# Optimization experiments

Hardware: AMD Instinct MI355X
Metric: run time of the kernel (lower is better)

The kernel has to match this reference:

```python
import jax, jax.numpy as jnp
import numpy as np

N = 4096
IN_F = 256
OUT_F = 128
K = 3
BETA = 0.5
ALPHA = 0.2  # leaky relu negative slope
NEG_BIG = -9e15


def setup_inputs() -> dict:
    key = jax.random.key(0)
    k1, k2, k3, k4 = jax.random.split(key, 4)
    h = jax.random.normal(k1, (N, IN_F), dtype=jnp.float32)
    k_mask_list = jax.random.randint(k2, (K, N, N), 0, 2, dtype=jnp.int32)
    # xavier_uniform with gain=1.414
    def xavier(k, shape, gain=1.414):
        fan_in, fan_out = shape[0], shape[1]
        bound = gain * np.sqrt(6.0 / (fan_in + fan_out))
        return jax.random.uniform(k, shape, jnp.float32, -bound, bound)
    W = xavier(k3, (IN_F * K, OUT_F))
    a = xavier(k4, (2 * OUT_F * K, 1))
    return {"h": h, "k_mask_list": k_mask_list, "W": W, "a": a}


def reference(h, k_mask_list, W, a):
    # dropout p=0.0 / eval mode -> identity
    Wh = None
    for i in range(K - 1, -1, -1):
        Whnew = h @ W[i * IN_F:(i + 1) * IN_F, :]              # [N, OUT_F]
        if i == K - 1:
            Wh = Whnew
        a1 = a[2 * i * OUT_F:(2 * i + 1) * OUT_F, :]           # [OUT_F, 1]
        a2 = a[(2 * i + 1) * OUT_F:(2 * i + 2) * OUT_F, :]     # [OUT_F, 1]
        Wh1 = Whnew @ a1                                        # [N, 1]
        Wh2 = Whnew @ a2                                        # [N, 1]
        e = jax.nn.leaky_relu(Wh1 + Wh2.T, negative_slope=ALPHA)  # [N, N]
        masked = jnp.where(k_mask_list[i] > 0, e, NEG_BIG)
        attention = jax.nn.softmax(masked, axis=1)              # [N, N]
        Wh = (1.0 - BETA) * (attention @ Whnew) + BETA * Wh
    return jax.nn.elu(Wh)  # concat=True
```

## Files before the change

### kernel.cpp

```cpp
#include <hip/hip_runtime.h>
#include <hip/hip_bf16.h>

#define NN 4096
#define IN_F 256
#define OUT_F 128
#define ALPHA 0.2f

typedef __bf16 bf16x8 __attribute__((ext_vector_type(8)));
typedef float f32x4 __attribute__((ext_vector_type(4)));
typedef float f32x16 __attribute__((ext_vector_type(16)));

__device__ __forceinline__ unsigned short f2bf(float f) {
  union { float f; unsigned int u; } x; x.f = f;
  unsigned int r = x.u + 0x7FFF + ((x.u >> 16) & 1);
  return (unsigned short)(r >> 16);
}

__global__ __launch_bounds__(256) void k_cvt_w(const float* __restrict__ W,
                                               unsigned short* __restrict__ Wtb) {
  const int i = blockIdx.y;
  const int k0 = blockIdx.x * 32;
  const int t = threadIdx.x;
  __shared__ float tile[32][129];
  #pragma unroll
  for (int j = 0; j < 16; ++j) {
    int idx = t + j * 256;
    int r = idx >> 7, c = idx & 127;
    tile[r][c] = W[(size_t)(i * IN_F + k0 + r) * OUT_F + c];
  }
  __syncthreads();
  const int c = t >> 1, half = t & 1;
  unsigned short* dst = Wtb + ((size_t)i * OUT_F + c) * IN_F + k0 + half * 16;
  #pragma unroll
  for (int g = 0; g < 4; ++g) {
    ushort4 v;
    v.x = f2bf(tile[half * 16 + g * 4 + 0][c]);
    v.y = f2bf(tile[half * 16 + g * 4 + 1][c]);
    v.z = f2bf(tile[half * 16 + g * 4 + 2][c]);
    v.w = f2bf(tile[half * 16 + g * 4 + 3][c]);
    *(ushort4*)(dst + g * 4) = v;
  }
}

__global__ __launch_bounds__(256) void k_front(const float* __restrict__ h,
                                               const unsigned short* __restrict__ Wtb,
                                               const float* __restrict__ a,
                                               float* __restrict__ Whnew2,
                                               unsigned short* __restrict__ Vopt,
                                               float* __restrict__ Wh1,
                                               float* __restrict__ Wh2,
                                               unsigned short* __restrict__ ew2pb,
                                               unsigned short* __restrict__ ew2mb,
                                               float* __restrict__ gmax2) {
  const int i = blockIdx.y;
  const int r0 = blockIdx.x * 32;
  const int t = threadIdx.x;
  const int lane = t & 63, wid = t >> 6;
  const int m = wid & 1, nh = wid >> 1, nbase = nh * 64;
  const int ln = lane & 15, lk = lane >> 4;

  __shared__ float a1s[128], a2s[128];
  __shared__ float red1[2][32], red2[2][32];
  __shared__ float ewsp[32], ewsm[32];
  __shared__ unsigned short T[2][32][130];

  if (t < 128) {
    a1s[t] = a[(size_t)2 * i * OUT_F + t];
    a2s[t] = a[(size_t)(2 * i + 1) * OUT_F + t];
  }
  __syncthreads();

  const float* ap = h + (size_t)(r0 + m * 16 + ln) * IN_F + lk * 8;
  const unsigned short* bp = Wtb + ((size_t)i * OUT_F + nbase + ln) * IN_F + lk * 8;

  f32x4 z4 = {0.f, 0.f, 0.f, 0.f};
  f32x4 acc[4] = {z4, z4, z4, z4};
  #pragma unroll
  for (int ks = 0; ks < 8; ++ks) {
    float4 h0 = *(const float4*)(ap + ks * 32);
    float4 h1 = *(const float4*)(ap + ks * 32 + 4);
    union { unsigned short u[8]; bf16x8 v; } av;
    av.u[0] = f2bf(h0.x); av.u[1] = f2bf(h0.y); av.u[2] = f2bf(h0.z); av.u[3] = f2bf(h0.w);
    av.u[4] = f2bf(h1.x); av.u[5] = f2bf(h1.y); av.u[6] = f2bf(h1.z); av.u[7] = f2bf(h1.w);
    acc[0] = __builtin_amdgcn_mfma_f32_16x16x32_bf16(av.v, *(const bf16x8*)(bp + 0 * 16 * IN_F + ks * 32), acc[0], 0, 0, 0);
    acc[1] = __builtin_amdgcn_mfma_f32_16x16x32_bf16(av.v, *(const bf16x8*)(bp + 1 * 16 * IN_F + ks * 32), acc[1], 0, 0, 0);
    acc[2] = __builtin_amdgcn_mfma_f32_16x16x32_bf16(av.v, *(const bf16x8*)(bp + 2 * 16 * IN_F + ks * 32), acc[2], 0, 0, 0);
    acc[3] = __builtin_amdgcn_mfma_f32_16x16x32_bf16(av.v, *(const bf16x8*)(bp + 3 * 16 * IN_F + ks * 32), acc[3], 0, 0, 0);
  }

  float d1[4] = {0.f, 0.f, 0.f, 0.f}, d2[4] = {0.f, 0.f, 0.f, 0.f};
  #pragma unroll
  for (int f = 0; f < 4; ++f) {
    const int col = nbase + f * 16 + ln;
    const float va1 = a1s[col], va2 = a2s[col];
    #pragma unroll
    for (int q = 0; q < 4; ++q) {
      const float v = acc[f][q];
      d1[q] += v * va1;
      d2[q] += v * va2;
    }
  }
  #pragma unroll
  for (int msk = 1; msk < 16; msk <<= 1) {
    #pragma unroll
    for (int q = 0; q < 4; ++q) {
      d1[q] += __shfl_xor(d1[q], msk, 64);
      d2[q] += __shfl_xor(d2[q], msk, 64);
    }
  }
  if (ln == 0) {
    #pragma unroll
    for (int q = 0; q < 4; ++q) {
      red1[nh][m * 16 + lk * 4 + q] = d1[q];
      red2[nh][m * 16 + lk * 4 + q] = d2[q];
    }
  }
  if (i == 2) {
    #pragma unroll
    for (int f = 0; f < 4; ++f) {
      const int col = nbase + f * 16 + ln;
      #pragma unroll
      for (int q = 0; q < 4; ++q)
        Whnew2[(size_t)(r0 + m * 16 + lk * 4 + q) * OUT_F + col] = acc[f][q];
    }
  }
  __syncthreads();

  if (t < 32) {
    const float w1 = red1[0][t] + red1[1][t];
    const float w2 = red2[0][t] + red2[1][t];
    Wh1[(size_t)i * NN + r0 + t] = w1;
    Wh2[(size_t)i * NN + r0 + t] = w2;
    const float ep = __expf(w2), em = __expf(ALPHA * w2);
    ewsp[t] = ep; ewsm[t] = em;
    ew2pb[(size_t)i * NN + r0 + t] = f2bf(ep);
    ew2mb[(size_t)i * NN + r0 + t] = f2bf(em);
    float mv = w2;
    #pragma unroll
    for (int o = 16; o > 0; o >>= 1) mv = fmaxf(mv, __shfl_down(mv, o, 32));
    if (t == 0 && mv > 0.f)
      atomicMax((int*)gmax2 + i, __float_as_int(mv));
  }
  __syncthreads();

  #pragma unroll
  for (int f = 0; f < 4; ++f) {
    const int n = nbase + f * 16 + ln;
    #pragma unroll
    for (int q = 0; q < 4; ++q) {
      const int c = m * 16 + lk * 4 + q;
      const float v = acc[f][q];
      T[0][c][n] = f2bf(ewsp[c] * v);
      T[1][c][n] = f2bf(ewsm[c] * v);
    }
  }
  __syncthreads();

  const int n = t & 127, ks = t >> 7;
  const int kslab = (r0 >> 4) + ks;
  #pragma unroll
  for (int s = 0; s < 2; ++s) {
    union { unsigned short u[16]; uint4 q[2]; } o;
    #pragma unroll
    for (int j = 0; j < 16; ++j) o.u[j] = T[s][ks * 16 + j][n];
    unsigned short* dst = Vopt + (((size_t)(i * 2 + s) * 256 + kslab) * 128 + n) * 16;
    *(uint4*)(dst) = o.q[0];
    *(uint4*)(dst + 8) = o.q[1];
  }
}

__global__ __launch_bounds__(256) void k_heavy(const unsigned short* __restrict__ Vopt,
                                               const int* __restrict__ mask,
                                               const float* __restrict__ Wh1,
                                               const float* __restrict__ Wh2,
                                               const unsigned short* __restrict__ ew2pb,
                                               const unsigned short* __restrict__ ew2mb,
                                               const float* __restrict__ gmax2,
                                               float* __restrict__ Upart,
                                               float* __restrict__ SPp,
                                               float* __restrict__ SMp) {
  const unsigned int lid = blockIdx.x + 64u * (blockIdx.y + 3u * blockIdx.z);
  const unsigned int swz = (lid & 7u) * 96u + (lid >> 3);
  const int bx = swz & 63;
  const int w = swz >> 6;
  const int i = w % 3;
  const int z = w / 3;

  const int r0 = bx * 64;
  const int cb = z * 1024;
  const int t = threadIdx.x, lane = t & 63, wid = t >> 6;
  const int m = wid & 1, nh = wid >> 1;
  const int l31 = lane & 31, kh = lane >> 5;
  const int n0 = nh * 64 + l31, n1 = n0 + 32;

  const int myrow = r0 + m * 32 + l31;
  const float w1 = Wh1[(size_t)i * NN + myrow];
  const int* mrow = mask + ((size_t)i * NN + myrow) * NN + cb + kh * 8;
  const float* w2p = Wh2 + (size_t)i * NN + cb + kh * 8;

  const size_t fragoff = (size_t)nh * 1024 + l31 * 16 + kh * 8;
  const unsigned short* vP = Vopt + ((size_t)(i * 2 + 0) * 256 + (cb >> 4)) * 2048 + fragoff;
  const unsigned short* vM = Vopt + ((size_t)(i * 2 + 1) * 256 + (cb >> 4)) * 2048 + fragoff;
  const unsigned short* eB = (nh == 0 ? ew2pb : ew2mb) + (size_t)i * NN + cb + kh * 8;

  f32x16 accP0 = {}, accP1 = {}, accM0 = {}, accM1 = {}, accS = {};

  #pragma unroll 2
  for (int kslab = 0; kslab < 64; ++kslab) {
    const int ks16 = kslab * 16;
    int4 ma = *(const int4*)(mrow + ks16);
    int4 mb = *(const int4*)(mrow + ks16 + 4);
    float4 wa = *(const float4*)(w2p + ks16);
    float4 wb = *(const float4*)(w2p + ks16 + 4);

    union { unsigned int u[4]; bf16x8 v; } aP, aM;
    {
      int mv[8] = {ma.x, ma.y, ma.z, ma.w, mb.x, mb.y, mb.z, mb.w};
      float wv[8] = {wa.x, wa.y, wa.z, wa.w, wb.x, wb.y, wb.z, wb.w};
      #pragma unroll
      for (int e = 0; e < 4; ++e) {
        const bool m0 = mv[2 * e] > 0,   p0 = (w1 + wv[2 * e]) > 0.f;
        const bool m1 = mv[2 * e + 1] > 0, p1 = (w1 + wv[2 * e + 1]) > 0.f;
        aP.u[e] = ((m0 && p0) ? 0x3F80u : 0u) | ((m1 && p1) ? 0x3F800000u : 0u);
        aM.u[e] = ((m0 && !p0) ? 0x3F80u : 0u) | ((m1 && !p1) ? 0x3F800000u : 0u);
      }
    }
    bf16x8 bP0 = *(const bf16x8*)(vP + (size_t)kslab * 2048);
    bf16x8 bP1 = *(const bf16x8*)(vP + (size_t)kslab * 2048 + 512);
    bf16x8 bM0 = *(const bf16x8*)(vM + (size_t)kslab * 2048);
    bf16x8 bM1 = *(const bf16x8*)(vM + (size_t)kslab * 2048 + 512);
    bf16x8 eF  = *(const bf16x8*)(eB + ks16);
    accP0 = __builtin_amdgcn_mfma_f32_32x32x16_bf16(aP.v, bP0, accP0, 0, 0, 0);
    accP1 = __builtin_amdgcn_mfma_f32_32x32x16_bf16(aP.v, bP1, accP1, 0, 0, 0);
    accM0 = __builtin_amdgcn_mfma_f32_32x32x16_bf16(aM.v, bM0, accM0, 0, 0, 0);
    accM1 = __builtin_amdgcn_mfma_f32_32x32x16_bf16(aM.v, bM1, accM1, 0, 0, 0);
    accS  = __builtin_amdgcn_mfma_f32_32x32x16_bf16(nh == 0 ? aP.v : aM.v, eF, accS, 0, 0, 0);
  }

  const float gi = gmax2[i];
  const int rbase = r0 + m * 32;
  #pragma unroll
  for (int q = 0; q < 16; ++q) {
    const int crow = (q & 3) + 8 * (q >> 2) + 4 * kh;
    const int r = rbase + crow;
    const float rw1 = Wh1[(size_t)i * NN + r];
    const float e0 = rw1 + gi;
    const float mx = (e0 > 0.f) ? e0 : ALPHA * e0;
    const float fp = __expf(rw1 - mx);
    const float fm = __expf(ALPHA * rw1 - mx);
    float* urow = Upart + ((size_t)(z * 3 + i) * NN + r) * OUT_F;
    urow[n0] = fp * accP0[q] + fm * accM0[q];
    urow[n1] = fp * accP1[q] + fm * accM1[q];
  }
  if (l31 == 0) {
    #pragma unroll
    for (int q = 0; q < 16; ++q) {
      const int r = rbase + (q & 3) + 8 * (q >> 2) + 4 * kh;
      if (nh == 0) SPp[(size_t)(z * 3 + i) * NN + r] = accS[q];
      else         SMp[(size_t)(z * 3 + i) * NN + r] = accS[q];
    }
  }
}

__global__ __launch_bounds__(256) void k_final(const float* __restrict__ Upart,
                                               const float* __restrict__ SPp,
                                               const float* __restrict__ SMp,
                                               const float* __restrict__ Wh1,
                                               const float* __restrict__ gmax2,
                                               const float* __restrict__ Whnew2,
                                               float* __restrict__ out) {
  int idx = blockIdx.x * 256 + threadIdx.x;
  int r = idx >> 7;
  float v = 0.125f * Whnew2[idx];
  #pragma unroll
  for (int i = 0; i < 3; ++i) {
    const float coef = (i == 0) ? 0.5f : (i == 1) ? 0.25f : 0.125f;
    const float w1 = Wh1[(size_t)i * NN + r];
    const float gi = gmax2[i];
    const float e0 = w1 + gi;
    const float mx = (e0 > 0.f) ? e0 : ALPHA * e0;
    const float fp = __expf(w1 - mx);
    const float fm = __expf(ALPHA * w1 - mx);
    float u = 0.f, sp = 0.f, sm = 0.f;
    #pragma unroll
    for (int zz = 0; zz < 4; ++zz) {
      u  += Upart[((size_t)(zz * 3 + i) * NN) * OUT_F + idx];
      sp += SPp[(size_t)(zz * 3 + i) * NN + r];
      sm += SMp[(size_t)(zz * 3 + i) * NN + r];
    }
    const float S = fp * sp + fm * sm;
    v += coef * u / S;
  }
  out[idx] = (v > 0.f) ? v : (__expf(v) - 1.0f);
}

extern "C" void kernel_launch(void* const* d_in, const int* in_sizes, int n_in,
                              void* d_out, int out_size, void* d_ws, size_t ws_size,
                              hipStream_t stream) {
  const float* h    = (const float*)d_in[0];
  const int*   mask = (const int*)d_in[1];
  const float* W    = (const float*)d_in[2];
  const float* a    = (const float*)d_in[3];
  float* out = (float*)d_out;

  float* Whnew2 = (float*)d_ws;
  float* Wh1    = Whnew2 + (size_t)NN * OUT_F;
  float* Wh2    = Wh1 + 3 * NN;
  float* gmax2  = Wh2 + 3 * NN;
  float* Upart  = gmax2 + 4;
  float* SPp    = Upart + (size_t)4 * 3 * NN * OUT_F;
  float* SMp    = SPp + 4 * 3 * NN;
  unsigned short* Wtb   = (unsigned short*)(SMp + 4 * 3 * NN);
  unsigned short* Vopt  = Wtb + (size_t)3 * OUT_F * IN_F;
  unsigned short* ew2pb = Vopt + (size_t)3 * 2 * 256 * 128 * 16;
  unsigned short* ew2mb = ew2pb + 3 * NN;

  hipMemsetAsync(gmax2, 0, 4 * sizeof(float), stream);
  k_cvt_w<<<dim3(8, 3), 256, 0, stream>>>(W, Wtb);
  k_front<<<dim3(128, 3), 256, 0, stream>>>(h, Wtb, a, Whnew2, Vopt, Wh1, Wh2, ew2pb, ew2mb, gmax2);
  k_heavy<<<dim3(64, 3, 4), 256, 0, stream>>>(Vopt, mask, Wh1, Wh2, ew2pb, ew2mb, gmax2, Upart, SPp, SMp);
  k_final<<<(NN * OUT_F) / 256, 256, 0, stream>>>(Upart, SPp, SMp, Wh1, gmax2, Whnew2, out);
}
```

Before: 398.0 us.

## Precompute mask sign bits cooperatively into LDS before MFMA loop

Each block now reads its 64x1024 mask tile once with coalesced row-wise loads. It computes the positive/negative leaky-relu selection as packed bits and stores them in shared memory. The MFMA loop then expands the bits into bf16 one-hot fragments from LDS. This removes duplicate mask reads by both column-half waves and the strided per-lane mask accesses. The cost is a serialized prologue with a barrier, so mask loading no longer overlaps with MFMA work.

```diff
diff --git a/kernel.cpp b/kernel.cpp
--- a/kernel.cpp
+++ b/kernel.cpp
@@ -14,6 +14,16 @@
   union { float f; unsigned int u; } x; x.f = f;
   unsigned int r = x.u + 0x7FFF + ((x.u >> 16) & 1);
   return (unsigned short)(r >> 16);
+}
+__device__ __forceinline__ bf16x8 bits2bf8(unsigned int b) {
+  union { unsigned int u[4]; bf16x8 v; } o;
+  #pragma unroll
+  for (int e = 0; e < 4; ++e) {
+    unsigned int lo = (b >> (2 * e)) & 1u;
+    unsigned int hi = (b >> (2 * e + 1)) & 1u;
+    o.u[e] = lo * 0x3F80u + hi * 0x3F800000u;
+  }
+  return o.v;
 }
 
 __global__ __launch_bounds__(256) void k_cvt_w(const float* __restrict__ W,
@@ -193,48 +203,62 @@
   const int l31 = lane & 31, kh = lane >> 5;
   const int n0 = nh * 64 + l31, n1 = n0 + 32;
 
-  const int myrow = r0 + m * 32 + l31;
-  const float w1 = Wh1[(size_t)i * NN + myrow];
-  const int* mrow = mask + ((size_t)i * NN + myrow) * NN + cb + kh * 8;
-  const float* w2p = Wh2 + (size_t)i * NN + cb + kh * 8;
+  __shared__ unsigned int bitsLDS[64][65];
+
+  const int wq = t >> 6;
+  const int cg = t & 63;
+  float w2v[16];
+  {
+    const float* w2b = Wh2 + (size_t)i * NN + cb + cg * 16;
+    #pragma unroll
+    for (int g = 0; g < 4; ++g) {
+      float4 f = *(const float4*)(w2b + g * 4);
+      w2v[g * 4 + 0] = f.x; w2v[g * 4 + 1] = f.y;
+      w2v[g * 4 + 2] = f.z; w2v[g * 4 + 3] = f.w;
+    }
+  }
+  const int* mcol = mask + ((size_t)i * NN + r0) * NN + cb + cg * 16;
+  #pragma unroll 2
+  for (int jj = 0; jj < 16; ++jj) {
+    const int rl = jj * 4 + wq;
+    const float w1r = Wh1[(size_t)i * NN + r0 + rl];
+    const int* mp = mcol + (size_t)rl * NN;
+    unsigned int bpk = 0, bmk = 0;
+    #pragma unroll
+    for (int g = 0; g < 4; ++g) {
+      int4 mv = *(const int4*)(mp + g * 4);
+      if (mv.x > 0) { if (w1r + w2v[g * 4 + 0] > 0.f) bpk |= 1u << (g * 4 + 0); else bmk |= 1u << (g * 4 + 0); }
+      if (mv.y > 0) { if (w1r + w2v[g * 4 + 1] > 0.f) bpk |= 1u << (g * 4 + 1); else bmk |= 1u << (g * 4 + 1); }
+      if (mv.z > 0) { if (w1r + w2v[g * 4 + 2] > 0.f) bpk |= 1u << (g * 4 + 2); else bmk |= 1u << (g * 4 + 2); }
+      if (mv.w > 0) { if (w1r + w2v[g * 4 + 3] > 0.f) bpk |= 1u << (g * 4 + 3); else bmk |= 1u << (g * 4 + 3); }
+    }
+    bitsLDS[rl][cg] = bpk | (bmk << 16);
+  }
+  __syncthreads();
 
   const size_t fragoff = (size_t)nh * 1024 + l31 * 16 + kh * 8;
   const unsigned short* vP = Vopt + ((size_t)(i * 2 + 0) * 256 + (cb >> 4)) * 2048 + fragoff;
   const unsigned short* vM = Vopt + ((size_t)(i * 2 + 1) * 256 + (cb >> 4)) * 2048 + fragoff;
   const unsigned short* eB = (nh == 0 ? ew2pb : ew2mb) + (size_t)i * NN + cb + kh * 8;
+  const int arow = m * 32 + l31;
 
   f32x16 accP0 = {}, accP1 = {}, accM0 = {}, accM1 = {}, accS = {};
 
   #pragma unroll 2
-  for (int kslab = 0; kslab < 64; ++kslab) {
-    const int ks16 = kslab * 16;
-    int4 ma = *(const int4*)(mrow + ks16);
-    int4 mb = *(const int4*)(mrow + ks16 + 4);
-    float4 wa = *(const float4*)(w2p + ks16);
-    float4 wb = *(const float4*)(w2p + ks16 + 4);
-
-    union { unsigned int u[4]; bf16x8 v; } aP, aM;
-    {
-      int mv[8] = {ma.x, ma.y, ma.z, ma.w, mb.x, mb.y, mb.z, mb.w};
-      float wv[8] = {wa.x, wa.y, wa.z, wa.w, wb.x, wb.y, wb.z, wb.w};
-      #pragma unroll
-      for (int e = 0; e < 4; ++e) {
-        const bool m0 = mv[2 * e] > 0,   p0 = (w1 + wv[2 * e]) > 0.f;
-        const bool m1 = mv[2 * e + 1] > 0, p1 = (w1 + wv[2 * e + 1]) > 0.f;
-        aP.u[e] = ((m0 && p0) ? 0x3F80u : 0u) | ((m1 && p1) ? 0x3F800000u : 0u);
-        aM.u[e] = ((m0 && !p0) ? 0x3F80u : 0u) | ((m1 && !p1) ? 0x3F800000u : 0u);
-      }
-    }
-    bf16x8 bP0 = *(const bf16x8*)(vP + (size_t)kslab * 2048);
-    bf16x8 bP1 = *(const bf16x8*)(vP + (size_t)kslab * 2048 + 512);
-    bf16x8 bM0 = *(const bf16x8*)(vM + (size_t)kslab * 2048);
-    bf16x8 bM1 = *(const bf16x8*)(vM + (size_t)kslab * 2048 + 512);
-    bf16x8 eF  = *(const bf16x8*)(eB + ks16);
-    accP0 = __builtin_amdgcn_mfma_f32_32x32x16_bf16(aP.v, bP0, accP0, 0, 0, 0);
-    accP1 = __builtin_amdgcn_mfma_f32_32x32x16_bf16(aP.v, bP1, accP1, 0, 0, 0);
-    accM0 = __builtin_amdgcn_mfma_f32_32x32x16_bf16(aM.v, bM0, accM0, 0, 0, 0);
-    accM1 = __builtin_amdgcn_mfma_f32_32x32x16_bf16(aM.v, bM1, accM1, 0, 0, 0);
-    accS  = __builtin_amdgcn_mfma_f32_32x32x16_bf16(nh == 0 ? aP.v : aM.v, eF, accS, 0, 0, 0);
+  for (int ks = 0; ks < 64; ++ks) {
+    const unsigned int wv = bitsLDS[arow][ks];
+    bf16x8 aP = bits2bf8((wv >> (kh * 8)) & 0xFFu);
+    bf16x8 aM = bits2bf8((wv >> (16 + kh * 8)) & 0xFFu);
+    bf16x8 bP0 = *(const bf16x8*)(vP + (size_t)ks * 2048);
+    bf16x8 bP1 = *(const bf16x8*)(vP + (size_t)ks * 2048 + 512);
+    bf16x8 bM0 = *(const bf16x8*)(vM + (size_t)ks * 2048);
+    bf16x8 bM1 = *(const bf16x8*)(vM + (size_t)ks * 2048 + 512);
+    bf16x8 eF  = *(const bf16x8*)(eB + ks * 16);
+    accP0 = __builtin_amdgcn_mfma_f32_32x32x16_bf16(aP, bP0, accP0, 0, 0, 0);
+    accP1 = __builtin_amdgcn_mfma_f32_32x32x16_bf16(aP, bP1, accP1, 0, 0, 0);
+    accM0 = __builtin_amdgcn_mfma_f32_32x32x16_bf16(aM, bM0, accM0, 0, 0, 0);
+    accM1 = __builtin_amdgcn_mfma_f32_32x32x16_bf16(aM, bM1, accM1, 0, 0, 0);
+    accS  = __builtin_amdgcn_mfma_f32_32x32x16_bf16(nh == 0 ? aP : aM, eF, accS, 0, 0, 0);
   }
 
   const float gi = gmax2[i];
```

Measured after the change: 396.7 us. No clear change (-0.3%).

## Precompute mask sign bits into LDS and stage V tiles with double buffering

Applied to the files above, without the earlier changes.

The heavy kernel now uses 512-thread blocks covering 128 rows by 512 columns. It first reads the int32 mask and the Wh1+Wh2 sign into a packed 8-bit-per-4-columns bit table in LDS, then streams the V slabs through double-buffered LDS staging shared by all warps instead of each warp loading them from global memory. The column split doubles to 8 partitions, so the final reduction and the workspace grow. This is meant to cut redundant global V loads and take mask decoding out of the MFMA loop, at the cost of extra syncthreads and more partial-sum traffic.

```diff
diff --git a/kernel.cpp b/kernel.cpp
--- a/kernel.cpp
+++ b/kernel.cpp
@@ -5,6 +5,8 @@
 #define IN_F 256
 #define OUT_F 128
 #define ALPHA 0.2f
+#define ROWS 128
+#define WCOLS 512
 
 typedef __bf16 bf16x8 __attribute__((ext_vector_type(8)));
 typedef float f32x4 __attribute__((ext_vector_type(4)));
@@ -169,76 +171,128 @@
   }
 }
 
-__global__ __launch_bounds__(256) void k_heavy(const unsigned short* __restrict__ Vopt,
-                                               const int* __restrict__ mask,
-                                               const float* __restrict__ Wh1,
-                                               const float* __restrict__ Wh2,
-                                               const unsigned short* __restrict__ ew2pb,
-                                               const unsigned short* __restrict__ ew2mb,
-                                               const float* __restrict__ gmax2,
-                                               float* __restrict__ Upart,
-                                               float* __restrict__ SPp,
-                                               float* __restrict__ SMp) {
-  const unsigned int lid = blockIdx.x + 64u * (blockIdx.y + 3u * blockIdx.z);
+__global__ __launch_bounds__(512, 4) void k_heavy(const unsigned short* __restrict__ Vopt,
+                                                  const int* __restrict__ mask,
+                                                  const float* __restrict__ Wh1,
+                                                  const float* __restrict__ Wh2,
+                                                  const unsigned short* __restrict__ ew2pb,
+                                                  const unsigned short* __restrict__ ew2mb,
+                                                  const float* __restrict__ gmax2,
+                                                  float* __restrict__ Upart,
+                                                  float* __restrict__ SPp,
+                                                  float* __restrict__ SMp) {
+  const unsigned int lid = blockIdx.x + 32u * (blockIdx.y + 3u * blockIdx.z);
   const unsigned int swz = (lid & 7u) * 96u + (lid >> 3);
-  const int bx = swz & 63;
-  const int w = swz >> 6;
+  const int bx = swz & 31;
+  const int w = swz >> 5;
   const int i = w % 3;
   const int z = w / 3;
 
-  const int r0 = bx * 64;
-  const int cb = z * 1024;
-  const int t = threadIdx.x, lane = t & 63, wid = t >> 6;
-  const int m = wid & 1, nh = wid >> 1;
+  const int r0 = bx * ROWS;
+  const int cb = z * WCOLS;
+  const int t = threadIdx.x;
+  const int lane = t & 63, wid = t >> 6;
+  const int g = wid & 3, nh = wid >> 2;
   const int l31 = lane & 31, kh = lane >> 5;
   const int n0 = nh * 64 + l31, n1 = n0 + 32;
 
-  const int myrow = r0 + m * 32 + l31;
-  const float w1 = Wh1[(size_t)i * NN + myrow];
-  const int* mrow = mask + ((size_t)i * NN + myrow) * NN + cb + kh * 8;
-  const float* w2p = Wh2 + (size_t)i * NN + cb + kh * 8;
-
-  const size_t fragoff = (size_t)nh * 1024 + l31 * 16 + kh * 8;
-  const unsigned short* vP = Vopt + ((size_t)(i * 2 + 0) * 256 + (cb >> 4)) * 2048 + fragoff;
-  const unsigned short* vM = Vopt + ((size_t)(i * 2 + 1) * 256 + (cb >> 4)) * 2048 + fragoff;
-  const unsigned short* eB = (nh == 0 ? ew2pb : ew2mb) + (size_t)i * NN + cb + kh * 8;
-
+  __shared__ unsigned char bits8[ROWS][132];
+  __shared__ unsigned short Vl[2][2][2][2048];
+  __shared__ unsigned short ews[2][WCOLS];
+
+  const int sg_st = wid >> 2;
+  const int q4 = wid & 3;
+  const unsigned short* myWin = Vopt + ((size_t)(i * 2 + sg_st) * 256 + (cb >> 4)) * 2048;
+  uint4 stg0, stg1;
+
+  {
+    const unsigned short* src = myWin + q4 * 1024 + lane * 8;
+    stg0 = *(const uint4*)(src);
+    stg1 = *(const uint4*)(src + 512);
+  }
+
+  if (t < WCOLS) {
+    ews[0][t] = ew2pb[(size_t)i * NN + cb + t];
+    ews[1][t] = ew2mb[(size_t)i * NN + cb + t];
+  }
+
+  {
+    const float* w2base = Wh2 + (size_t)i * NN + cb;
+    float4 w2a = *(const float4*)(w2base + lane * 4);
+    float4 w2b = *(const float4*)(w2base + 256 + lane * 4);
+    const int* mbase = mask + ((size_t)i * NN + r0) * NN + cb;
+    for (int p = 0; p < 16; ++p) {
+      const int r = p * 8 + wid;
+      const float w1 = Wh1[(size_t)i * NN + r0 + r];
+      const int* mp = mbase + (size_t)r * NN;
+      int4 ma = *(const int4*)(mp + lane * 4);
+      int4 mb = *(const int4*)(mp + 256 + lane * 4);
+      unsigned int b0 = 0, b1 = 0;
+      if (ma.x > 0) { if (w1 + w2a.x > 0.f) b0 |= 1u;  else b0 |= 16u; }
+      if (ma.y > 0) { if (w1 + w2a.y > 0.f) b0 |= 2u;  else b0 |= 32u; }
+      if (ma.z > 0) { if (w1 + w2a.z > 0.f) b0 |= 4u;  else b0 |= 64u; }
+      if (ma.w > 0) { if (w1 + w2a.w > 0.f) b0 |= 8u;  else b0 |= 128u; }
+      if (mb.x > 0) { if (w1 + w2b.x > 0.f) b1 |= 1u;  else b1 |= 16u; }
+      if (mb.y > 0) { if (w1 + w2b.y > 0.f) b1 |= 2u;  else b1 |= 32u; }
+      if (mb.z > 0) { if (w1 + w2b.z > 0.f) b1 |= 4u;  else b1 |= 64u; }
+      if (mb.w > 0) { if (w1 + w2b.w > 0.f) b1 |= 8u;  else b1 |= 128u; }
+      bits8[r][lane] = (unsigned char)b0;
+      bits8[r][64 + lane] = (unsigned char)b1;
+    }
+  }
+
+  __syncthreads();
+  {
+    unsigned short* dst = &Vl[0][sg_st][0][0] + q4 * 1024 + lane * 8;
+    *(uint4*)dst = stg0;
+    *(uint4*)(dst + 512) = stg1;
+  }
+  __syncthreads();
+
+  const int arow = g * 32 + l31;
   f32x16 accP0 = {}, accP1 = {}, accM0 = {}, accM1 = {}, accS = {};
 
-  #pragma unroll 2
-  for (int kslab = 0; kslab < 64; ++kslab) {
-    const int ks16 = kslab * 16;
-    int4 ma = *(const int4*)(mrow + ks16);
-    int4 mb = *(const int4*)(mrow + ks16 + 4);
-    float4 wa = *(const float4*)(w2p + ks16);
-    float4 wb = *(const float4*)(w2p + ks16 + 4);
-
-    union { unsigned int u[4]; bf16x8 v; } aP, aM;
-    {
-      int mv[8] = {ma.x, ma.y, ma.z, ma.w, mb.x, mb.y, mb.z, mb.w};
-      float wv[8] = {wa.x, wa.y, wa.z, wa.w, wb.x, wb.y, wb.z, wb.w};
+  for (int c = 0; c < 16; ++c) {
+    if (c < 15) {
+      const unsigned short* src = myWin + (size_t)(c + 1) * 4096 + q4 * 1024 + lane * 8;
+      stg0 = *(const uint4*)(src);
+      stg1 = *(const uint4*)(src + 512);
+    }
+    const int buf = c & 1;
+    #pragma unroll
+    for (int sc = 0; sc < 2; ++sc) {
+      const int s = 2 * c + sc;
+      const unsigned int w32 = *(const unsigned int*)&bits8[arow][s * 4];
+      const unsigned int hw = (w32 >> (kh * 16)) & 0xFFFFu;
+      union { unsigned int u[4]; bf16x8 v; } aP, aM;
       #pragma unroll
       for (int e = 0; e < 4; ++e) {
-        const bool m0 = mv[2 * e] > 0,   p0 = (w1 + wv[2 * e]) > 0.f;
-        const bool m1 = mv[2 * e + 1] > 0, p1 = (w1 + wv[2 * e + 1]) > 0.f;
-        aP.u[e] = ((m0 && p0) ? 0x3F80u : 0u) | ((m1 && p1) ? 0x3F800000u : 0u);
-        aM.u[e] = ((m0 && !p0) ? 0x3F80u : 0u) | ((m1 && !p1) ? 0x3F800000u : 0u);
+        const int base = 2 * e + ((e >> 1) << 2);
+        aP.u[e] = ((hw >> base) & 1u) * 0x3F80u + ((hw >> (base + 1)) & 1u) * 0x3F800000u;
+        aM.u[e] = ((hw >> (base + 4)) & 1u) * 0x3F80u + ((hw >> (base + 5)) & 1u) * 0x3F800000u;
       }
-    }
-    bf16x8 bP0 = *(const bf16x8*)(vP + (size_t)kslab * 2048);
-    bf16x8 bP1 = *(const bf16x8*)(vP + (size_t)kslab * 2048 + 512);
-    bf16x8 bM0 = *(const bf16x8*)(vM + (size_t)kslab * 2048);
-    bf16x8 bM1 = *(const bf16x8*)(vM + (size_t)kslab * 2048 + 512);
-    bf16x8 eF  = *(const bf16x8*)(eB + ks16);
-    accP0 = __builtin_amdgcn_mfma_f32_32x32x16_bf16(aP.v, bP0, accP0, 0, 0, 0);
-    accP1 = __builtin_amdgcn_mfma_f32_32x32x16_bf16(aP.v, bP1, accP1, 0, 0, 0);
-    accM0 = __builtin_amdgcn_mfma_f32_32x32x16_bf16(aM.v, bM0, accM0, 0, 0, 0);
-    accM1 = __builtin_amdgcn_mfma_f32_32x32x16_bf16(aM.v, bM1, accM1, 0, 0, 0);
-    accS  = __builtin_amdgcn_mfma_f32_32x32x16_bf16(nh == 0 ? aP.v : aM.v, eF, accS, 0, 0, 0);
+      bf16x8 bP0 = *(const bf16x8*)&Vl[buf][0][sc][n0 * 16 + kh * 8];
+      bf16x8 bP1 = *(const bf16x8*)&Vl[buf][0][sc][n1 * 16 + kh * 8];
+      bf16x8 bM0 = *(const bf16x8*)&Vl[buf][1][sc][n0 * 16 + kh * 8];
+      bf16x8 bM1 = *(const bf16x8*)&Vl[buf][1][sc][n1 * 16 + kh * 8];
+      bf16x8 eF  = *(const bf16x8*)&ews[nh][s * 16 + kh * 8];
+      accP0 = __builtin_amdgcn_mfma_f32_32x32x16_bf16(aP.v, bP0, accP0, 0, 0, 0);
+      accP1 = __builtin_amdgcn_mfma_f32_32x32x16_bf16(aP.v, bP1, accP1, 0, 0, 0);
+      accM0 = __builtin_amdgcn_mfma_f32_32x32x16_bf16(aM.v, bM0, accM0, 0, 0, 0);
+      accM1 = __builtin_amdgcn_mfma_f32_32x32x16_bf16(aM.v, bM1, accM1, 0, 0, 0);
+      accS  = __builtin_amdgcn_mfma_f32_32x32x16_bf16(nh == 0 ? aP.v : aM.v, eF, accS, 0, 0, 0);
+    }
+    if (c < 15) {
+      __syncthreads();
+      unsigned short* dst = &Vl[buf ^ 1][sg_st][0][0] + q4 * 1024 + lane * 8;
+      *(uint4*)dst = stg0;
+      *(uint4*)(dst + 512) = stg1;
+      __syncthreads();
+    }
   }
 
   const float gi = gmax2[i];
-  const int rbase = r0 + m * 32;
+  const int rbase = r0 + g * 32;
   #pragma unroll
   for (int q = 0; q < 16; ++q) {
     const int crow = (q & 3) + 8 * (q >> 2) + 4 * kh;
@@ -283,7 +337,7 @@
     const float fm = __expf(ALPHA * w1 - mx);
     float u = 0.f, sp = 0.f, sm = 0.f;
     #pragma unroll
-    for (int zz = 0; zz < 4; ++zz) {
+    for (int zz = 0; zz < 8; ++zz) {
       u  += Upart[((size_t)(zz * 3 + i) * NN) * OUT_F + idx];
       sp += SPp[(size_t)(zz * 3 + i) * NN + r];
       sm += SMp[(size_t)(zz * 3 + i) * NN + r];
@@ -308,9 +362,9 @@
   float* Wh2    = Wh1 + 3 * NN;
   float* gmax2  = Wh2 + 3 * NN;
   float* Upart  = gmax2 + 4;
-  float* SPp    = Upart + (size_t)4 * 3 * NN * OUT_F;
-  float* SMp    = SPp + 4 * 3 * NN;
-  unsigned short* Wtb   = (unsigned short*)(SMp + 4 * 3 * NN);
+  float* SPp    = Upart + (size_t)8 * 3 * NN * OUT_F;
+  float* SMp    = SPp + 8 * 3 * NN;
+  unsigned short* Wtb   = (unsigned short*)(SMp + 8 * 3 * NN);
   unsigned short* Vopt  = Wtb + (size_t)3 * OUT_F * IN_F;
   unsigned short* ew2pb = Vopt + (size_t)3 * 2 * 256 * 128 * 16;
   unsigned short* ew2mb = ew2pb + 3 * NN;
@@ -318,6 +372,6 @@
   hipMemsetAsync(gmax2, 0, 4 * sizeof(float), stream);
   k_cvt_w<<<dim3(8, 3), 256, 0, stream>>>(W, Wtb);
   k_front<<<dim3(128, 3), 256, 0, stream>>>(h, Wtb, a, Whnew2, Vopt, Wh1, Wh2, ew2pb, ew2mb, gmax2);
-  k_heavy<<<dim3(64, 3, 4), 256, 0, stream>>>(Vopt, mask, Wh1, Wh2, ew2pb, ew2mb, gmax2, Upart, SPp, SMp);
+  k_heavy<<<dim3(32, 3, 8), 512, 0, stream>>>(Vopt, mask, Wh1, Wh2, ew2pb, ew2mb, gmax2, Upart, SPp, SMp);
   k_final<<<(NN * OUT_F) / 256, 256, 0, stream>>>(Upart, SPp, SMp, Wh1, gmax2, Whnew2, out);
 }
```

Result: faster. 346.6 us (-12.9%).
